# Performance work log

Hardware: AMD Instinct MI355X
Metric: run time of the kernel (lower is better)

Reference implementation:

```python
import jax, jax.numpy as jnp
import numpy as np

H1 = 51  # lstm1 hidden size
H2 = 1   # lstm2 hidden size


def _lstm_cell(x, h, c, Wih, Whh, bih, bhh):
    # PyTorch LSTMCell: gates = x W_ih^T + b_ih + h W_hh^T + b_hh, order i,f,g,o
    gates = x @ Wih.T + h @ Whh.T + (bih + bhh)
    i, f, g, o = jnp.split(gates, 4, axis=-1)
    i = jax.nn.sigmoid(i)
    f = jax.nn.sigmoid(f)
    g = jnp.tanh(g)
    o = jax.nn.sigmoid(o)
    c_new = f * c + i * g
    h_new = o * jnp.tanh(c_new)
    return h_new, c_new


def setup_inputs() -> dict:
    key = jax.random.key(0)
    ks = jax.random.split(key, 9)
    B, T = 2048, 1024
    s1 = 1.0 / np.sqrt(H1)
    s2 = 1.0 / np.sqrt(H2)
    u = lambda k, shape, s: jax.random.uniform(k, shape, jnp.float32, -s, s)
    return {
        "input": jax.random.normal(ks[0], (B, T), dtype=jnp.float32),
        "W_ih1": u(ks[1], (4 * H1, 1), s1),
        "W_hh1": u(ks[2], (4 * H1, H1), s1),
        "b_ih1": u(ks[3], (4 * H1,), s1),
        "b_hh1": u(ks[4], (4 * H1,), s1),
        "W_ih2": u(ks[5], (4 * H2, H1), s2),
        "W_hh2": u(ks[6], (4 * H2, H2), s2),
        "b_ih2": u(ks[7], (4 * H2,), s2),
        "b_hh2": u(ks[8], (4 * H2,), s2),
        "future": 64,
    }


def reference(input, W_ih1, W_hh1, b_ih1, b_hh1, W_ih2, W_hh2, b_ih2, b_hh2, future):
    B = input.shape[0]
    dt = input.dtype
    h1 = jnp.zeros((B, H1), dt)
    c1 = jnp.zeros((B, H1), dt)
    h2 = jnp.zeros((B, H2), dt)
    c2 = jnp.zeros((B, H2), dt)

    def step(carry, x_t):
        h1, c1, h2, c2 = carry
        h1, c1 = _lstm_cell(x_t, h1, c1, W_ih1, W_hh1, b_ih1, b_hh1)
        h2, c2 = _lstm_cell(h1, h2, c2, W_ih2, W_hh2, b_ih2, b_hh2)
        return (h1, c1, h2, c2), h2

    xs = jnp.swapaxes(input, 0, 1)[:, :, None]  # [T, B, 1]
    carry, outs = jax.lax.scan(step, (h1, c1, h2, c2), xs)

    def step_future(carry, _):
        h1, c1, h2, c2 = carry
        h1, c1 = _lstm_cell(h2, h1, c1, W_ih1, W_hh1, b_ih1, b_hh1)
        h2, c2 = _lstm_cell(h1, h2, c2, W_ih2, W_hh2, b_ih2, b_hh2)
        return (h1, c1, h2, c2), h2

    if future > 0:
        _, outs_f = jax.lax.scan(step_future, carry, None, length=future)
        outs = jnp.concatenate([outs, outs_f], axis=0)

    # [T+F, B, 1] -> [B, T+F]
    return jnp.swapaxes(outs[:, :, 0], 0, 1)
```

## Files before the change

kernel.cpp:

```cpp
#include <hip/hip_runtime.h>


#define H1N  51
#define NP   26
#define WAVE 64

typedef float v2f __attribute__((ext_vector_type(2)));

#define INV_LN2   1.44269504088896340736f
#define INV_LN2X2 2.88539008177792681472f

__device__ __forceinline__ float sigmoid_s(float xs) {
    return __builtin_amdgcn_rcpf(1.0f + __builtin_amdgcn_exp2f(-xs));
}
__device__ __forceinline__ float tanh_s2(float xs2) {
    float e = __builtin_amdgcn_exp2f(xs2);
    return fmaf(-2.0f, __builtin_amdgcn_rcpf(e + 1.0f), 1.0f);
}
__device__ __forceinline__ float tanh_nat(float x) {
    return tanh_s2(x * INV_LN2X2);
}
__device__ __forceinline__ float rdlane(float v, int k) {
    return __int_as_float(__builtin_amdgcn_readlane(__float_as_int(v), k));
}

__global__ __attribute__((amdgpu_flat_work_group_size(64, 64),
                          amdgpu_waves_per_eu(1, 1)))
void lstm_seq2(const float* __restrict__ input,
               const float* __restrict__ W_ih1,
               const float* __restrict__ W_hh1,
               const float* __restrict__ b_ih1,
               const float* __restrict__ b_hh1,
               const float* __restrict__ W_ih2,
               const float* __restrict__ W_hh2,
               const float* __restrict__ b_ih2,
               const float* __restrict__ b_hh2,
               float* __restrict__ out,
               int T, int TF)
{
    const int j   = threadIdx.x;
    const bool jv = (j < H1N);
    const int jj  = jv ? j : 0;
    const float m = jv ? 1.0f : 0.0f;
    const bool isz = (j >= H1N) && (j < H1N + 4);
    const int  q   = isz ? (j - H1N) : 0;
    const float mz = isz ? 1.0f : 0.0f;
    const float s2q = (q == 2) ? INV_LN2X2 : INV_LN2;

    const int sA = 2 * blockIdx.x, sB = sA + 1;

    const int r_i = jj, r_f = H1N + jj, r_g = 2*H1N + jj, r_o = 3*H1N + jj;
    const float s_i = INV_LN2, s_f = INV_LN2, s_g = INV_LN2X2, s_o = INV_LN2;

    v2f wI[NP], wF[NP], wG[NP], wO[NP];
#pragma unroll
    for (int kk = 0; kk < NP; ++kk) {
        const int k0 = 2*kk, k1 = k0 + 1;
        wI[kk].x = m*s_i*W_hh1[r_i*H1N + k0] + mz*s2q*W_ih2[q*H1N + k0];
        wF[kk].x = m*s_f*W_hh1[r_f*H1N + k0];
        wG[kk].x = m*s_g*W_hh1[r_g*H1N + k0];
        wO[kk].x = m*s_o*W_hh1[r_o*H1N + k0];
        if (k1 < H1N) {
            wI[kk].y = m*s_i*W_hh1[r_i*H1N + k1] + mz*s2q*W_ih2[q*H1N + k1];
            wF[kk].y = m*s_f*W_hh1[r_f*H1N + k1];
            wG[kk].y = m*s_g*W_hh1[r_g*H1N + k1];
            wO[kk].y = m*s_o*W_hh1[r_o*H1N + k1];
        } else {
            wI[kk].y = m*s_i*(b_ih1[r_i] + b_hh1[r_i]);
            wF[kk].y = m*s_f*(b_ih1[r_f] + b_hh1[r_f]);
            wG[kk].y = m*s_g*(b_ih1[r_g] + b_hh1[r_g]);
            wO[kk].y = m*s_o*(b_ih1[r_o] + b_hh1[r_o]);
        }
    }
#pragma unroll
    for (int kk = 0; kk < NP; ++kk)
        asm volatile("" : "+v"(wI[kk]), "+v"(wF[kk]), "+v"(wG[kk]), "+v"(wO[kk]));

    const float wx_i = m*s_i*W_ih1[r_i];
    const float wx_f = m*s_f*W_ih1[r_f];
    const float wx_g = m*s_g*W_ih1[r_g];
    const float wx_o = m*s_o*W_ih1[r_o];

    const float wh2_0 = INV_LN2*W_hh2[0], wh2_1 = INV_LN2*W_hh2[1];
    const float wh2_2 = INV_LN2X2*W_hh2[2], wh2_3 = INV_LN2*W_hh2[3];
    const float b2_0 = INV_LN2*(b_ih2[0] + b_hh2[0]), b2_1 = INV_LN2*(b_ih2[1] + b_hh2[1]);
    const float b2_2 = INV_LN2X2*(b_ih2[2] + b_hh2[2]), b2_3 = INV_LN2*(b_ih2[3] + b_hh2[3]);

    __shared__ __align__(16) float hrowA[WAVE];
    __shared__ __align__(16) float hrowB[WAVE];
    __shared__ __align__(16) float zbA[4];
    __shared__ __align__(16) float zbB[4];
    hrowA[j] = (j == H1N) ? 1.0f : 0.0f;
    hrowB[j] = (j == H1N) ? 1.0f : 0.0f;

    float c1A = 0.0f, h2A = 0.0f, c2A = 0.0f;
    float c1B = 0.0f, h2B = 0.0f, c2B = 0.0f;

    const float* __restrict__ xrowA = input + (long)sA * T;
    const float* __restrict__ xrowB = input + (long)sB * T;
    float* __restrict__ orowA = out + (long)sA * TF;
    float* __restrict__ orowB = out + (long)sB * TF;

    float xbufA = 0.0f, xbufB = 0.0f, obufA = 0.0f, obufB = 0.0f;

    auto phase = [&](int sel, float& c1, float& h2, float& c2, float& obuf,
                     float xin, int xmode, int do_l2, int do_fin, int tt) {
        float* hrow = sel ? hrowB : hrowA;
        float* zb   = sel ? zbB   : zbA;
        v2f aI = {0.0f, 0.0f}, aF = {0.0f, 0.0f};
        v2f aG = {0.0f, 0.0f}, aO = {0.0f, 0.0f};
#pragma unroll
        for (int kk = 0; kk < NP; ++kk) {
            const v2f hp = *(const v2f*)&hrow[2*kk];
            asm("v_pk_fma_f32 %0, %4, %8, %0\n\t"
                "v_pk_fma_f32 %1, %5, %8, %1\n\t"
                "v_pk_fma_f32 %2, %6, %8, %2\n\t"
                "v_pk_fma_f32 %3, %7, %8, %3"
                : "+v"(aI), "+v"(aF), "+v"(aG), "+v"(aO)
                : "v"(wI[kk]), "v"(wF[kk]), "v"(wG[kk]), "v"(wO[kk]), "v"(hp));
        }
        const float mI = aI.x + aI.y;
        if (isz) zb[q] = mI;
        const float mF = aF.x + aF.y, mG = aG.x + aG.y, mO = aO.x + aO.y;

        if (do_l2) {
            const float4 z = *(const float4*)zb;
            const float g2i = sigmoid_s(fmaf(wh2_0, h2, b2_0 + z.x));
            const float g2f = sigmoid_s(fmaf(wh2_1, h2, b2_1 + z.y));
            const float g2g = tanh_s2 (fmaf(wh2_2, h2, b2_2 + z.z));
            const float g2o = sigmoid_s(fmaf(wh2_3, h2, b2_3 + z.w));
            c2 = fmaf(g2f, c2, g2i * g2g);
            h2 = g2o * tanh_nat(c2);
            obuf = (j == (tt & 63)) ? h2 : obuf;
        }
        if (do_fin) {
            const float x = (xmode == 0) ? xin : h2;
            const float gi = sigmoid_s(fmaf(wx_i, x, mI));
            const float gf = sigmoid_s(fmaf(wx_f, x, mF));
            const float gg = tanh_s2 (fmaf(wx_g, x, mG));
            const float go = sigmoid_s(fmaf(wx_o, x, mO));
            c1 = fmaf(gf, c1, gi * gg);
            const float h1 = go * tanh_nat(c1);
            if (jv) hrow[j] = h1;
        }
    };

    xbufA = xrowA[j]; xbufB = xrowB[j];
    phase(0, c1A, h2A, c2A, obufA, rdlane(xbufA, 0), 0, 0, 1, 0);
    phase(1, c1B, h2B, c2B, obufB, rdlane(xbufB, 0), 0, 0, 1, 0);

    for (int n = 1; n < T; ++n) {
        if ((n & 63) == 0) { xbufA = xrowA[n + j]; xbufB = xrowB[n + j]; }
        const int u = n & 63;
        const float xA = rdlane(xbufA, u), xB = rdlane(xbufB, u);
        phase(0, c1A, h2A, c2A, obufA, xA, 0, 1, 1, n - 1);
        phase(1, c1B, h2B, c2B, obufB, xB, 0, 1, 1, n - 1);
        if ((n & 63) == 0) {
            orowA[n - 64 + j] = obufA;
            orowB[n - 64 + j] = obufB;
        }
    }

    phase(0, c1A, h2A, c2A, obufA, 0.0f, 1, 1, 1, T - 1);
    phase(1, c1B, h2B, c2B, obufB, 0.0f, 1, 1, 1, T - 1);
    orowA[T - 64 + j] = obufA;
    orowB[T - 64 + j] = obufB;

    for (int n = T + 1; n < TF; ++n) {
        phase(0, c1A, h2A, c2A, obufA, 0.0f, 1, 1, 1, n - 1);
        phase(1, c1B, h2B, c2B, obufB, 0.0f, 1, 1, 1, n - 1);
    }

    phase(0, c1A, h2A, c2A, obufA, 0.0f, 1, 1, 0, TF - 1);
    phase(1, c1B, h2B, c2B, obufB, 0.0f, 1, 1, 0, TF - 1);
    orowA[TF - 64 + j] = obufA;
    orowB[TF - 64 + j] = obufB;
}

extern "C" void kernel_launch(void* const* d_in, const int* in_sizes, int n_in,
                              void* d_out, int out_size, void* d_ws, size_t ws_size,
                              hipStream_t stream) {
    const float* input = (const float*)d_in[0];
    const float* W_ih1 = (const float*)d_in[1];
    const float* W_hh1 = (const float*)d_in[2];
    const float* b_ih1 = (const float*)d_in[3];
    const float* b_hh1 = (const float*)d_in[4];
    const float* W_ih2 = (const float*)d_in[5];
    const float* W_hh2 = (const float*)d_in[6];
    const float* b_ih2 = (const float*)d_in[7];
    const float* b_hh2 = (const float*)d_in[8];
    float* out = (float*)d_out;

    const int B  = 2048;
    const int T  = in_sizes[0] / B;
    const int TF = out_size   / B;

    lstm_seq2<<<dim3(B / 2), dim3(WAVE), 0, stream>>>(
        input, W_ih1, W_hh1, b_ih1, b_hh1, W_ih2, W_hh2, b_ih2, b_hh2,
        out, T, TF);
}
```

Before: 1.267 ms.

## Run one sequence per wave, move g/o gate weights to shared LDS

Each wave now processes a single batch row instead of interleaving two, with four waves per block. Half of the recurrent weights (g and o gates) move from registers into LDS shared by the block, which cuts register pressure so two waves can run per EU. The aim is latency hiding across waves instead of ILP within one wave. The cost is extra LDS reads of the g/o weights on every timestep of the dot product.

```diff
diff --git a/kernel.cpp b/kernel.cpp
--- a/kernel.cpp
+++ b/kernel.cpp
@@ -4,6 +4,8 @@
 #define H1N  51
 #define NP   26
 #define WAVE 64
+#define WPB  4
+#define WST  54
 
 typedef float v2f __attribute__((ext_vector_type(2)));
 
@@ -24,9 +26,9 @@
     return __int_as_float(__builtin_amdgcn_readlane(__float_as_int(v), k));
 }
 
-__global__ __attribute__((amdgpu_flat_work_group_size(64, 64),
-                          amdgpu_waves_per_eu(1, 1)))
-void lstm_seq2(const float* __restrict__ input,
+__global__ __attribute__((amdgpu_flat_work_group_size(256, 256),
+                          amdgpu_waves_per_eu(2)))
+void lstm_seq1(const float* __restrict__ input,
                const float* __restrict__ W_ih1,
                const float* __restrict__ W_hh1,
                const float* __restrict__ b_ih1,
@@ -38,7 +40,9 @@
                float* __restrict__ out,
                int T, int TF)
 {
-    const int j   = threadIdx.x;
+    const int tid = threadIdx.x;
+    const int j   = tid & (WAVE - 1);
+    const int wid = tid >> 6;
     const bool jv = (j < H1N);
     const int jj  = jv ? j : 0;
     const float m = jv ? 1.0f : 0.0f;
@@ -47,34 +51,51 @@
     const float mz = isz ? 1.0f : 0.0f;
     const float s2q = (q == 2) ? INV_LN2X2 : INV_LN2;
 
-    const int sA = 2 * blockIdx.x, sB = sA + 1;
+    const int s = blockIdx.x * WPB + wid;
 
     const int r_i = jj, r_f = H1N + jj, r_g = 2*H1N + jj, r_o = 3*H1N + jj;
     const float s_i = INV_LN2, s_f = INV_LN2, s_g = INV_LN2X2, s_o = INV_LN2;
 
-    v2f wI[NP], wF[NP], wG[NP], wO[NP];
+    __shared__ __align__(16) float wlds[2][WAVE][WST];
+    __shared__ __align__(16) float hrow[WPB][WAVE];
+    __shared__ __align__(16) float zbs[WPB][4];
+
+    v2f wI[NP], wF[NP];
 #pragma unroll
     for (int kk = 0; kk < NP; ++kk) {
         const int k0 = 2*kk, k1 = k0 + 1;
         wI[kk].x = m*s_i*W_hh1[r_i*H1N + k0] + mz*s2q*W_ih2[q*H1N + k0];
         wF[kk].x = m*s_f*W_hh1[r_f*H1N + k0];
-        wG[kk].x = m*s_g*W_hh1[r_g*H1N + k0];
-        wO[kk].x = m*s_o*W_hh1[r_o*H1N + k0];
         if (k1 < H1N) {
             wI[kk].y = m*s_i*W_hh1[r_i*H1N + k1] + mz*s2q*W_ih2[q*H1N + k1];
             wF[kk].y = m*s_f*W_hh1[r_f*H1N + k1];
-            wG[kk].y = m*s_g*W_hh1[r_g*H1N + k1];
-            wO[kk].y = m*s_o*W_hh1[r_o*H1N + k1];
         } else {
             wI[kk].y = m*s_i*(b_ih1[r_i] + b_hh1[r_i]);
             wF[kk].y = m*s_f*(b_ih1[r_f] + b_hh1[r_f]);
-            wG[kk].y = m*s_g*(b_ih1[r_g] + b_hh1[r_g]);
-            wO[kk].y = m*s_o*(b_ih1[r_o] + b_hh1[r_o]);
         }
     }
 #pragma unroll
     for (int kk = 0; kk < NP; ++kk)
-        asm volatile("" : "+v"(wI[kk]), "+v"(wF[kk]), "+v"(wG[kk]), "+v"(wO[kk]));
+        asm volatile("" : "+v"(wI[kk]), "+v"(wF[kk]));
+
+    if (tid < WAVE) {
+#pragma unroll
+        for (int kk = 0; kk < NP; ++kk) {
+            const int k0 = 2*kk, k1 = k0 + 1;
+            const float g0 = m*s_g*W_hh1[r_g*H1N + k0];
+            const float o0 = m*s_o*W_hh1[r_o*H1N + k0];
+            float g1, o1;
+            if (k1 < H1N) {
+                g1 = m*s_g*W_hh1[r_g*H1N + k1];
+                o1 = m*s_o*W_hh1[r_o*H1N + k1];
+            } else {
+                g1 = m*s_g*(b_ih1[r_g] + b_hh1[r_g]);
+                o1 = m*s_o*(b_ih1[r_o] + b_hh1[r_o]);
+            }
+            wlds[0][j][k0] = g0; wlds[0][j][k0+1] = g1;
+            wlds[1][j][k0] = o0; wlds[1][j][k0+1] = o1;
+        }
+    }
 
     const float wx_i = m*s_i*W_ih1[r_i];
     const float wx_f = m*s_f*W_ih1[r_f];
@@ -86,45 +107,42 @@
     const float b2_0 = INV_LN2*(b_ih2[0] + b_hh2[0]), b2_1 = INV_LN2*(b_ih2[1] + b_hh2[1]);
     const float b2_2 = INV_LN2X2*(b_ih2[2] + b_hh2[2]), b2_3 = INV_LN2*(b_ih2[3] + b_hh2[3]);
 
-    __shared__ __align__(16) float hrowA[WAVE];
-    __shared__ __align__(16) float hrowB[WAVE];
-    __shared__ __align__(16) float zbA[4];
-    __shared__ __align__(16) float zbB[4];
-    hrowA[j] = (j == H1N) ? 1.0f : 0.0f;
-    hrowB[j] = (j == H1N) ? 1.0f : 0.0f;
-
-    float c1A = 0.0f, h2A = 0.0f, c2A = 0.0f;
-    float c1B = 0.0f, h2B = 0.0f, c2B = 0.0f;
-
-    const float* __restrict__ xrowA = input + (long)sA * T;
-    const float* __restrict__ xrowB = input + (long)sB * T;
-    float* __restrict__ orowA = out + (long)sA * TF;
-    float* __restrict__ orowB = out + (long)sB * TF;
-
-    float xbufA = 0.0f, xbufB = 0.0f, obufA = 0.0f, obufB = 0.0f;
-
-    auto phase = [&](int sel, float& c1, float& h2, float& c2, float& obuf,
-                     float xin, int xmode, int do_l2, int do_fin, int tt) {
-        float* hrow = sel ? hrowB : hrowA;
-        float* zb   = sel ? zbB   : zbA;
+    hrow[wid][j] = (j == H1N) ? 1.0f : 0.0f;
+    __syncthreads();
+
+    float* __restrict__ hw  = hrow[wid];
+    float* __restrict__ zbw = zbs[wid];
+    const float* __restrict__ wgt = &wlds[0][j][0];
+    const float* __restrict__ wot = &wlds[1][j][0];
+
+    float c1 = 0.0f, h2 = 0.0f, c2 = 0.0f;
+
+    const float* __restrict__ xrow = input + (long)s * T;
+    float* __restrict__ orow = out + (long)s * TF;
+
+    float xbuf = 0.0f, obuf = 0.0f;
+
+    auto phase = [&](float xin, int xmode, int do_l2, int do_fin, int tt) {
         v2f aI = {0.0f, 0.0f}, aF = {0.0f, 0.0f};
         v2f aG = {0.0f, 0.0f}, aO = {0.0f, 0.0f};
 #pragma unroll
         for (int kk = 0; kk < NP; ++kk) {
-            const v2f hp = *(const v2f*)&hrow[2*kk];
+            const v2f hp = *(const v2f*)&hw[2*kk];
+            const v2f gk = *(const v2f*)&wgt[2*kk];
+            const v2f ok = *(const v2f*)&wot[2*kk];
             asm("v_pk_fma_f32 %0, %4, %8, %0\n\t"
                 "v_pk_fma_f32 %1, %5, %8, %1\n\t"
                 "v_pk_fma_f32 %2, %6, %8, %2\n\t"
                 "v_pk_fma_f32 %3, %7, %8, %3"
                 : "+v"(aI), "+v"(aF), "+v"(aG), "+v"(aO)
-                : "v"(wI[kk]), "v"(wF[kk]), "v"(wG[kk]), "v"(wO[kk]), "v"(hp));
+                : "v"(wI[kk]), "v"(wF[kk]), "v"(gk), "v"(ok), "v"(hp));
         }
         const float mI = aI.x + aI.y;
-        if (isz) zb[q] = mI;
+        if (isz) zbw[q] = mI;
         const float mF = aF.x + aF.y, mG = aG.x + aG.y, mO = aO.x + aO.y;
 
         if (do_l2) {
-            const float4 z = *(const float4*)zb;
+            const float4 z = *(const float4*)zbw;
             const float g2i = sigmoid_s(fmaf(wh2_0, h2, b2_0 + z.x));
             const float g2f = sigmoid_s(fmaf(wh2_1, h2, b2_1 + z.y));
             const float g2g = tanh_s2 (fmaf(wh2_2, h2, b2_2 + z.z));
@@ -141,40 +159,28 @@
             const float go = sigmoid_s(fmaf(wx_o, x, mO));
             c1 = fmaf(gf, c1, gi * gg);
             const float h1 = go * tanh_nat(c1);
-            if (jv) hrow[j] = h1;
+            if (jv) hw[j] = h1;
         }
     };
 
-    xbufA = xrowA[j]; xbufB = xrowB[j];
-    phase(0, c1A, h2A, c2A, obufA, rdlane(xbufA, 0), 0, 0, 1, 0);
-    phase(1, c1B, h2B, c2B, obufB, rdlane(xbufB, 0), 0, 0, 1, 0);
+    xbuf = xrow[j];
+    phase(rdlane(xbuf, 0), 0, 0, 1, 0);
 
     for (int n = 1; n < T; ++n) {
-        if ((n & 63) == 0) { xbufA = xrowA[n + j]; xbufB = xrowB[n + j]; }
-        const int u = n & 63;
-        const float xA = rdlane(xbufA, u), xB = rdlane(xbufB, u);
-        phase(0, c1A, h2A, c2A, obufA, xA, 0, 1, 1, n - 1);
-        phase(1, c1B, h2B, c2B, obufB, xB, 0, 1, 1, n - 1);
-        if ((n & 63) == 0) {
-            orowA[n - 64 + j] = obufA;
-            orowB[n - 64 + j] = obufB;
-        }
+        if ((n & 63) == 0) xbuf = xrow[n + j];
+        const float x = rdlane(xbuf, n & 63);
+        phase(x, 0, 1, 1, n - 1);
+        if ((n & 63) == 0) orow[n - 64 + j] = obuf;
     }
 
-    phase(0, c1A, h2A, c2A, obufA, 0.0f, 1, 1, 1, T - 1);
-    phase(1, c1B, h2B, c2B, obufB, 0.0f, 1, 1, 1, T - 1);
-    orowA[T - 64 + j] = obufA;
-    orowB[T - 64 + j] = obufB;
-
-    for (int n = T + 1; n < TF; ++n) {
-        phase(0, c1A, h2A, c2A, obufA, 0.0f, 1, 1, 1, n - 1);
-        phase(1, c1B, h2B, c2B, obufB, 0.0f, 1, 1, 1, n - 1);
-    }
-
-    phase(0, c1A, h2A, c2A, obufA, 0.0f, 1, 1, 0, TF - 1);
-    phase(1, c1B, h2B, c2B, obufB, 0.0f, 1, 1, 0, TF - 1);
-    orowA[TF - 64 + j] = obufA;
-    orowB[TF - 64 + j] = obufB;
+    phase(0.0f, 1, 1, 1, T - 1);
+    orow[T - 64 + j] = obuf;
+
+    for (int n = T + 1; n < TF; ++n)
+        phase(0.0f, 1, 1, 1, n - 1);
+
+    phase(0.0f, 1, 1, 0, TF - 1);
+    orow[TF - 64 + j] = obuf;
 }
 
 extern "C" void kernel_launch(void* const* d_in, const int* in_sizes, int n_in,
@@ -195,7 +201,7 @@
     const int T  = in_sizes[0] / B;
     const int TF = out_size   / B;
 
-    lstm_seq2<<<dim3(B / 2), dim3(WAVE), 0, stream>>>(
+    lstm_seq1<<<dim3(B / WPB), dim3(WPB * WAVE), 0, stream>>>(
         input, W_ih1, W_hh1, b_ih1, b_hh1, W_ih2, W_hh2, b_ih2, b_hh2,
         out, T, TF);
 }
```

After: 1.210 ms. 4.5% less time.
